# Performance work log

Hardware: AMD Instinct MI355X
Metric: run time of the kernel (lower is better)

The kernel has to match this reference:

```python
import jax, jax.numpy as jnp
import numpy as np

TEMPERATURE = 0.07
EPS = 1e-8  # torch F.cosine_similarity eps


def setup_inputs() -> dict:
    key = jax.random.key(0)
    k1, k2 = jax.random.split(key)
    N, D = 4096, 256
    z1 = jax.random.normal(k1, (N, D), dtype=jnp.float32)
    z2 = jax.random.normal(k2, (N, D), dtype=jnp.float32)
    return {"z1": z1, "z2": z2}


def reference(z1, z2):
    N = z1.shape[0]
    z = jnp.concatenate([z1, z2], axis=0)  # (2N, D)
    # cosine similarity = normalize(z) @ normalize(z).T (with eps clamp on norms)
    norms = jnp.maximum(jnp.linalg.norm(z, axis=-1, keepdims=True), EPS)
    zn = z / norms
    sim = (zn @ zn.T) / TEMPERATURE  # (2N, 2N)
    twoN = 2 * N
    eye = jnp.eye(twoN, dtype=bool)
    sim = jnp.where(eye, -1e9, sim)
    pos = jnp.concatenate([jnp.arange(N, twoN), jnp.arange(0, N)])
    # cross entropy with integer targets, mean reduction
    logZ = jax.nn.logsumexp(sim, axis=-1)  # (2N,)
    pos_logit = jnp.take_along_axis(sim, pos[:, None], axis=1)[:, 0]
    loss = jnp.mean(logZ - pos_logit)
    return loss
```

## Files before the change

### kernel.cpp

```cpp
#include <hip/hip_runtime.h>

#define N2   8192
#define DDIM 256
#define NTRI 2080

static constexpr float INV_T = 1.0f / 0.07f;

using f32x4 = __attribute__((ext_vector_type(4))) float;
typedef unsigned int  u32;
typedef long long     i64;

#define GL2LDS(gp, lp) __builtin_amdgcn_global_load_lds( \
    (const __attribute__((address_space(1))) void*)(gp), \
    (__attribute__((address_space(3))) void*)(lp), 16, 0, 0)

__global__ void ntx_norm(const float* __restrict__ z1, const float* __restrict__ z2,
                         unsigned char* __restrict__ zn)
{
    const int w    = threadIdx.x >> 6;
    const int lane = threadIdx.x & 63;
    const int row  = blockIdx.x * 4 + w;

    const float* src = (row < 4096) ? (z1 + (size_t)row * DDIM)
                                    : (z2 + (size_t)(row - 4096) * DDIM);
    float4 v = *(const float4*)(src + lane * 4);
    float ss = v.x * v.x + v.y * v.y + v.z * v.z + v.w * v.w;
    #pragma unroll
    for (int m = 1; m < 64; m <<= 1) ss += __shfl_xor(ss, m, 64);

    float inv = 1.0f / fmaxf(sqrtf(ss), 1e-8f);

    u32 p = __builtin_amdgcn_cvt_pk_fp8_f32(v.x * inv, v.y * inv, 0u, false);
    p     = __builtin_amdgcn_cvt_pk_fp8_f32(v.z * inv, v.w * inv, p, true);
    ((u32*)zn)[(size_t)row * 64 + lane] = p;
}

__global__ __launch_bounds__(256, 3)
void ntx_gemm(const unsigned char* __restrict__ zn, float* __restrict__ partials,
              float* __restrict__ pos)
{
    __shared__ unsigned char lsA[16384];
    __shared__ unsigned char lsB[16384];

    const int tid  = threadIdx.x;
    const int lane = tid & 63;
    const int w    = tid >> 6;
    const int wr   = w >> 1;
    const int wc   = w & 1;

    const int t = (int)blockIdx.x;
    int br = (int)((129.0f - sqrtf(16641.0f - 8.0f * (float)t)) * 0.5f);
    while ((br + 1) * (129 - (br + 1)) / 2 <= t) ++br;
    while (br * (129 - br) / 2 > t) --br;
    const int bc = br + (t - br * (129 - br) / 2);

    const int fr  = lane & 15;
    const int kl  = lane >> 4;
    const int swz = (fr & 3) << 4;

    auto stage = [&](int kt) {
        #pragma unroll
        for (int i = 0; i < 4; ++i) {
            const int row = i * 32 + w * 8 + (lane >> 3);
            const int sc  = ((lane & 7) * 16) ^ ((row & 3) << 4);
            GL2LDS((const char*)zn + (size_t)(br * 128 + row) * 256 + kt * 128 + sc,
                   (unsigned char*)lsA + i * 4096 + w * 1024);
            GL2LDS((const char*)zn + (size_t)(bc * 128 + row) * 256 + kt * 128 + sc,
                   (unsigned char*)lsB + i * 4096 + w * 1024);
        }
    };

    f32x4 acc[4][4] = {};

    auto compute = [&]() {
        #pragma unroll
        for (int ks = 0; ks < 4; ++ks) {
            const int kb = ks * 32 + kl * 8;
            i64 af[4], bv[4];
            #pragma unroll
            for (int mf = 0; mf < 4; ++mf) {
                const int r = wr * 64 + mf * 16 + fr;
                af[mf] = *(const i64*)((const char*)lsA + r * 128 + (kb ^ swz));
            }
            #pragma unroll
            for (int nf = 0; nf < 4; ++nf) {
                const int c = wc * 64 + nf * 16 + fr;
                bv[nf] = *(const i64*)((const char*)lsB + c * 128 + (kb ^ swz));
            }
            __builtin_amdgcn_s_setprio(1);
            #pragma unroll
            for (int mf = 0; mf < 4; ++mf)
                #pragma unroll
                for (int nf = 0; nf < 4; ++nf)
                    acc[mf][nf] = __builtin_amdgcn_mfma_f32_16x16x32_fp8_fp8(
                        af[mf], bv[nf], acc[mf][nf], 0, 0, 0);
            __builtin_amdgcn_s_setprio(0);
        }
    };

    stage(0);
    __syncthreads();
    compute();
    __syncthreads();
    stage(1);
    __syncthreads();
    compute();

    const bool offdiag = (br != bc);
    const bool posblk  = (bc == br + 32);
    float colsum[4] = {0.f, 0.f, 0.f, 0.f};

    #pragma unroll
    for (int mf = 0; mf < 4; ++mf) {
        float rs[4] = {0.f, 0.f, 0.f, 0.f};
        const int rowq = br * 128 + wr * 64 + mf * 16 + kl * 4;
        #pragma unroll
        for (int nf = 0; nf < 4; ++nf) {
            const int col = bc * 128 + wc * 64 + nf * 16 + fr;
            f32x4 a = acc[mf][nf];
            #pragma unroll
            for (int j = 0; j < 4; ++j) {
                float e = (rowq + j == col) ? 0.f : __expf((a[j] - 1.0f) * INV_T);
                rs[j]      += e;
                colsum[nf] += e;
                if (posblk && (rowq + j + 4096 == col)) {
                    pos[rowq + j] = a[j];
                    pos[col]      = a[j];
                }
            }
        }
        #pragma unroll
        for (int m = 1; m < 16; m <<= 1) {
            #pragma unroll
            for (int j = 0; j < 4; ++j) rs[j] += __shfl_xor(rs[j], m, 64);
        }
        if (fr == 0) {
            float* p = partials + (size_t)rowq * 128 + bc * 2 + wc;
            p[0]   = rs[0];
            p[128] = rs[1];
            p[256] = rs[2];
            p[384] = rs[3];
        }
    }

    if (offdiag) {
        #pragma unroll
        for (int m = 16; m < 64; m <<= 1) {
            #pragma unroll
            for (int nf = 0; nf < 4; ++nf) colsum[nf] += __shfl_xor(colsum[nf], m, 64);
        }
        if (kl == 0) {
            #pragma unroll
            for (int nf = 0; nf < 4; ++nf) {
                const int col = bc * 128 + wc * 64 + nf * 16 + fr;
                partials[(size_t)col * 128 + br * 2 + wr] = colsum[nf];
            }
        }
    }
}

__global__ void ntx_loss(const float* __restrict__ partials, const float* __restrict__ pos,
                         float* __restrict__ bsums, u32* __restrict__ counter,
                         float* __restrict__ out)
{
    __shared__ float sm[16];
    __shared__ u32 flag;
    const int tid  = threadIdx.x;
    const int lane = tid & 63;
    const int w    = tid >> 6;

    float a = 0.f;
    #pragma unroll
    for (int i = 0; i < 8; ++i) {
        const int row = blockIdx.x * 128 + w * 8 + i;
        float S = partials[(size_t)row * 128 + lane] + partials[(size_t)row * 128 + 64 + lane];
        #pragma unroll
        for (int m = 1; m < 64; m <<= 1) S += __shfl_xor(S, m, 64);
        if (lane == 0) a += __logf(S) + INV_T - pos[row] * INV_T;
    }
    if (lane == 0) sm[w] = a;
    __syncthreads();

    if (tid == 0) {
        float b = 0.f;
        #pragma unroll
        for (int i = 0; i < 16; ++i) b += sm[i];
        bsums[blockIdx.x] = b;
        __threadfence();
        u32 old = atomicAdd(counter, 1u);
        flag = (old == 63u) ? 1u : 0u;
    }
    __syncthreads();

    if (flag && w == 0) {
        __threadfence();
        float v = bsums[lane];
        #pragma unroll
        for (int m = 1; m < 64; m <<= 1) v += __shfl_xor(v, m, 64);
        if (lane == 0) out[0] = v * (1.0f / (float)N2);
    }
}

extern "C" void kernel_launch(void* const* d_in, const int* in_sizes, int n_in,
                              void* d_out, int out_size, void* d_ws, size_t ws_size,
                              hipStream_t stream)
{
    const float* z1 = (const float*)d_in[0];
    const float* z2 = (const float*)d_in[1];
    float* out = (float*)d_out;

    unsigned char* zn       = (unsigned char*)d_ws;
    float*         partials = (float*)((char*)d_ws + (2u << 20));
    float*         pos      = (float*)((char*)d_ws + (6u << 20));
    float*         bsums    = pos + N2;
    u32*           counter  = (u32*)(bsums + 64);

    hipMemsetAsync(counter, 0, 4, stream);
    ntx_norm<<<N2 / 4, 256, 0, stream>>>(z1, z2, zn);
    ntx_gemm<<<NTRI, 256, 0, stream>>>(zn, partials, pos);
    ntx_loss<<<64, 1024, 0, stream>>>(partials, pos, bsums, counter, out);
}
```

Measured before the change: 55.21 us.

## Use scaled 16x16x128 FP8 MFMA with 128-bit LDS loads and wider swizzle

Replaces the four 16x16x32 FP8 MFMAs per k-tile with a single gfx950 scaled 16x16x128 f8f6f4 MFMA that uses unit scales. Fragments are now read from LDS as two 16-byte vector loads instead of 8-byte loads. The XOR swizzle is widened to 8 rows so the wider reads avoid bank conflicts. Staging address math is hoisted out of the loop. This cuts MFMA issue count and LDS instructions, but depends on the new k-layout and swizzle matching the one used at staging.

```diff
diff --git a/kernel.cpp b/kernel.cpp
--- a/kernel.cpp
+++ b/kernel.cpp
@@ -1,19 +1,21 @@
 #include <hip/hip_runtime.h>
 
 #define N2   8192
-#define DDIM 256
 #define NTRI 2080
 
 static constexpr float INV_T = 1.0f / 0.07f;
 
 using f32x4 = __attribute__((ext_vector_type(4))) float;
-typedef unsigned int  u32;
-typedef long long     i64;
+using i32x4 = __attribute__((ext_vector_type(4))) int;
+using i32x8 = __attribute__((ext_vector_type(8))) int;
+typedef unsigned int u32;
 
 #define GL2LDS(gp, lp) __builtin_amdgcn_global_load_lds( \
     (const __attribute__((address_space(1))) void*)(gp), \
     (__attribute__((address_space(3))) void*)(lp), 16, 0, 0)
 
+#define SCALE1 0x7F7F7F7F
+
 __global__ void ntx_norm(const float* __restrict__ z1, const float* __restrict__ z2,
                          unsigned char* __restrict__ zn)
 {
@@ -21,8 +23,8 @@
     const int lane = threadIdx.x & 63;
     const int row  = blockIdx.x * 4 + w;
 
-    const float* src = (row < 4096) ? (z1 + (size_t)row * DDIM)
-                                    : (z2 + (size_t)(row - 4096) * DDIM);
+    const float* src = (row < 4096) ? (z1 + (size_t)row * 256)
+                                    : (z2 + (size_t)(row - 4096) * 256);
     float4 v = *(const float4*)(src + lane * 4);
     float ss = v.x * v.x + v.y * v.y + v.z * v.z + v.w * v.w;
     #pragma unroll
@@ -39,8 +41,8 @@
 void ntx_gemm(const unsigned char* __restrict__ zn, float* __restrict__ partials,
               float* __restrict__ pos)
 {
-    __shared__ unsigned char lsA[16384];
-    __shared__ unsigned char lsB[16384];
+    __shared__ __align__(16) unsigned char lsA[16384];
+    __shared__ __align__(16) unsigned char lsB[16384];
 
     const int tid  = threadIdx.x;
     const int lane = tid & 63;
@@ -56,46 +58,50 @@
 
     const int fr  = lane & 15;
     const int kl  = lane >> 4;
-    const int swz = (fr & 3) << 4;
+    const int swz = (fr & 7) << 4;
+
+    const int srow = w * 8 + (lane >> 3);
+    const int scsw = ((lane & 7) * 16) ^ ((lane >> 3) << 4);
 
     auto stage = [&](int kt) {
+        const char* gA = (const char*)zn + (size_t)(br * 128 + srow) * 256 + kt * 128 + scsw;
+        const char* gB = (const char*)zn + (size_t)(bc * 128 + srow) * 256 + kt * 128 + scsw;
         #pragma unroll
         for (int i = 0; i < 4; ++i) {
-            const int row = i * 32 + w * 8 + (lane >> 3);
-            const int sc  = ((lane & 7) * 16) ^ ((row & 3) << 4);
-            GL2LDS((const char*)zn + (size_t)(br * 128 + row) * 256 + kt * 128 + sc,
-                   (unsigned char*)lsA + i * 4096 + w * 1024);
-            GL2LDS((const char*)zn + (size_t)(bc * 128 + row) * 256 + kt * 128 + sc,
-                   (unsigned char*)lsB + i * 4096 + w * 1024);
+            GL2LDS(gA + (size_t)i * 8192, lsA + i * 4096 + w * 1024);
+            GL2LDS(gB + (size_t)i * 8192, lsB + i * 4096 + w * 1024);
         }
     };
 
     f32x4 acc[4][4] = {};
 
     auto compute = [&]() {
-        #pragma unroll
-        for (int ks = 0; ks < 4; ++ks) {
-            const int kb = ks * 32 + kl * 8;
-            i64 af[4], bv[4];
-            #pragma unroll
-            for (int mf = 0; mf < 4; ++mf) {
-                const int r = wr * 64 + mf * 16 + fr;
-                af[mf] = *(const i64*)((const char*)lsA + r * 128 + (kb ^ swz));
-            }
-            #pragma unroll
-            for (int nf = 0; nf < 4; ++nf) {
-                const int c = wc * 64 + nf * 16 + fr;
-                bv[nf] = *(const i64*)((const char*)lsB + c * 128 + (kb ^ swz));
-            }
-            __builtin_amdgcn_s_setprio(1);
-            #pragma unroll
-            for (int mf = 0; mf < 4; ++mf)
-                #pragma unroll
-                for (int nf = 0; nf < 4; ++nf)
-                    acc[mf][nf] = __builtin_amdgcn_mfma_f32_16x16x32_fp8_fp8(
-                        af[mf], bv[nf], acc[mf][nf], 0, 0, 0);
-            __builtin_amdgcn_s_setprio(0);
-        }
+        const int kb = kl * 32;
+        i32x8 af[4], bv[4];
+        #pragma unroll
+        for (int mf = 0; mf < 4; ++mf) {
+            const int r = wr * 64 + mf * 16 + fr;
+            const char* base = (const char*)lsA + r * 128;
+            i32x4 lo = *(const i32x4*)(base + ((kb)      ^ swz));
+            i32x4 hi = *(const i32x4*)(base + ((kb + 16) ^ swz));
+            af[mf] = (i32x8){lo[0], lo[1], lo[2], lo[3], hi[0], hi[1], hi[2], hi[3]};
+        }
+        #pragma unroll
+        for (int nf = 0; nf < 4; ++nf) {
+            const int c = wc * 64 + nf * 16 + fr;
+            const char* base = (const char*)lsB + c * 128;
+            i32x4 lo = *(const i32x4*)(base + ((kb)      ^ swz));
+            i32x4 hi = *(const i32x4*)(base + ((kb + 16) ^ swz));
+            bv[nf] = (i32x8){lo[0], lo[1], lo[2], lo[3], hi[0], hi[1], hi[2], hi[3]};
+        }
+        __builtin_amdgcn_s_setprio(1);
+        #pragma unroll
+        for (int mf = 0; mf < 4; ++mf)
+            #pragma unroll
+            for (int nf = 0; nf < 4; ++nf)
+                acc[mf][nf] = __builtin_amdgcn_mfma_scale_f32_16x16x128_f8f6f4(
+                    af[mf], bv[nf], acc[mf][nf], 0, 0, 0, SCALE1, 0, SCALE1);
+        __builtin_amdgcn_s_setprio(0);
     };
 
     stage(0);
```

Measured after the change: 48.14 us. 1.15x faster.
